# Optimization experiments

Hardware: AMD Instinct MI355X
Metric: run time of the kernel (lower is better)

## Reference

```python
import jax, jax.numpy as jnp
import numpy as np
from jax.scipy.special import logsumexp

UNK_ID = 1
B, T, V = 128, 33, 25000
E, H, D = 256, 256, 512
N, C = 8192, 16384
L = T - 1


def setup_inputs() -> dict:
    key = jax.random.key(0)
    ks = jax.random.split(key, 12)
    input_memories = jax.random.normal(ks[0], (N, D), jnp.float32)
    # each target owns a contiguous block of N//B memories (every segment non-empty)
    origin = jnp.repeat(jnp.arange(B, dtype=jnp.int32), N // B)
    initial_states = jax.random.normal(ks[1], (B, H), jnp.float32)
    target_token_ids = jax.random.randint(ks[2], (B, T), 0, V)
    # copyable elements: pick (memory n, time l); flat idx into [N,L] and [B,L]
    mem_pick = jax.random.randint(ks[3], (C,), 0, N)
    t_pick = jax.random.randint(ks[4], (C,), 0, L)
    copyable_elements_idxs = mem_pick * L + t_pick
    copyable_elements_sample_idxs = origin[mem_pick] * L + t_pick
    target_lengths = jax.random.randint(ks[5], (B,), 1, L + 1)
    emb_weight = 0.02 * jax.random.normal(ks[6], (V, E), jnp.float32)
    gru_w_ih = 0.05 * jax.random.normal(ks[7], (3 * H, E), jnp.float32)
    gru_w_hh = 0.05 * jax.random.normal(ks[8], (3 * H, H), jnp.float32)
    gru_b_ih = jnp.zeros((3 * H,), jnp.float32)
    gru_b_hh = jnp.zeros((3 * H,), jnp.float32)
    w_std_att = 0.05 * jax.random.normal(ks[9], (H, D), jnp.float32)
    w_copy_att = 0.05 * jax.random.normal(ks[10], (H, D), jnp.float32)
    hidden_to_vocab = 0.01 * jax.random.normal(ks[11], (2 * H, E), jnp.float32)
    vocab_bias = jnp.zeros((V,), jnp.float32)
    return dict(input_memories=input_memories, input_memories_origin_idx=origin,
                initial_states=initial_states, target_token_ids=target_token_ids,
                copyable_elements_idxs=copyable_elements_idxs,
                copyable_elements_sample_idxs=copyable_elements_sample_idxs,
                target_lengths=target_lengths, emb_weight=emb_weight,
                gru_w_ih=gru_w_ih, gru_w_hh=gru_w_hh, gru_b_ih=gru_b_ih,
                gru_b_hh=gru_b_hh, w_std_att=w_std_att, w_copy_att=w_copy_att,
                hidden_to_vocab=hidden_to_vocab, vocab_bias=vocab_bias)


def _gru(x, h0, w_ih, w_hh, b_ih, b_hh):
    # x: [B,L,E], h0: [B,H] -> outputs [B,L,H], last state [B,H]
    def step(h, xt):
        gi = xt @ w_ih.T + b_ih
        gh = h @ w_hh.T + b_hh
        ir, iz, inew = jnp.split(gi, 3, axis=-1)
        hr, hz, hnew = jnp.split(gh, 3, axis=-1)
        r = jax.nn.sigmoid(ir + hr)
        z = jax.nn.sigmoid(iz + hz)
        n = jnp.tanh(inew + r * hnew)
        h_next = (1.0 - z) * n + z * h
        return h_next, h_next
    h_last, ys = jax.lax.scan(step, h0, jnp.swapaxes(x, 0, 1))
    return jnp.swapaxes(ys, 0, 1), h_last


def _seg_log_softmax(x, idx, num_seg):
    m = jax.ops.segment_max(x, idx, num_segments=num_seg)
    x_sh = x - m[idx]
    s = jax.ops.segment_sum(jnp.exp(x_sh), idx, num_segments=num_seg)
    return x_sh - jnp.log(s)[idx]


def _seg_logsumexp(x, idx, num_seg):
    m = jax.ops.segment_max(x, idx, num_segments=num_seg)
    m_safe = jnp.where(jnp.isfinite(m), m, 0.0)
    s = jax.ops.segment_sum(jnp.exp(x - m_safe[idx]), idx, num_segments=num_seg)
    return jnp.where(s > 0, jnp.log(jnp.where(s > 0, s, 1.0)) + m_safe, -jnp.inf)


def reference(input_memories, input_memories_origin_idx, initial_states,
              target_token_ids, copyable_elements_idxs,
              copyable_elements_sample_idxs, target_lengths, emb_weight,
              gru_w_ih, gru_w_hh, gru_b_ih, gru_b_hh, w_std_att, w_copy_att,
              hidden_to_vocab, vocab_bias):
    origin = input_memories_origin_idx
    b, t = target_token_ids.shape
    l = t - 1
    tok_in = target_token_ids[:, :-1]
    tok_out = target_token_ids[:, 1:]

    x = emb_weight[tok_in]                                   # [B,L,E]
    out_states, _ = _gru(x, initial_states, gru_w_ih, gru_w_hh, gru_b_ih, gru_b_hh)
    std_reps = input_memories @ w_std_att.T                  # [N,H]
    copy_reps = input_memories @ w_copy_att.T                # [N,H]
    out_per_input = out_states[origin]                       # [N,L,H]
    std_scores = jnp.einsum('nlh,nh->nl', out_per_input, std_reps)
    copy_scores = jnp.einsum('nlh,nh->nl', out_per_input, copy_reps)

    std_logprobs = _seg_log_softmax(std_scores, origin, b)   # [N,L]
    std_mul = jnp.exp(std_logprobs)[:, :, None] * std_reps[:, None, :]
    std_out = jax.ops.segment_sum(std_mul, origin, num_segments=b)  # [B,L,H]

    cat = jnp.concatenate([std_out, out_states], axis=-1)    # [B,L,2H]
    target_scores = (cat @ hidden_to_vocab) @ emb_weight.T + vocab_bias  # [B,L,V]

    total_copy = _seg_logsumexp(copy_scores, origin, b)      # [B,L]
    all_scores = jnp.concatenate([target_scores, total_copy[:, :, None]], axis=-1)
    norm = logsumexp(all_scores, axis=-1)                    # [B,L]
    target_logprobs = target_scores - norm[:, :, None]
    copy_logprobs = copy_scores - norm[origin]               # [N,L]

    num_valid = jax.ops.segment_sum(jnp.ones_like(copyable_elements_sample_idxs),
                                    copyable_elements_sample_idxs,
                                    num_segments=b * l)
    valid_copy = num_valid.reshape(b, l) > 0
    unk_loc = tok_out == UNK_ID
    mask = valid_copy & unk_loc

    gen_lp = jnp.take_along_axis(target_logprobs, tok_out[:, :, None], axis=-1)[..., 0]
    gen_lp = jnp.where(mask, -jnp.inf, gen_lp)

    cc = _seg_logsumexp(copy_logprobs.reshape(-1)[copyable_elements_idxs],
                        copyable_elements_sample_idxs, b * l).reshape(b, l)

    any_lp = logsumexp(jnp.stack([gen_lp, cc]), axis=0)      # [B,L]
    len_mask = (jnp.arange(l)[None, :] < target_lengths[:, None]).astype(jnp.float32)
    per_seq = (any_lp * len_mask).sum(-1) / len_mask.sum(-1)
    return -per_seq.mean()
```

## Files before the change

### kernel.cpp

```cpp
#include <hip/hip_runtime.h>
#include <hip/hip_bf16.h>

#define UNK 1
constexpr int B  = 128, T = 33, V = 25000, E = 256, H = 256, D = 512;
constexpr int N  = 8192, C = 16384, L = 32;
constexpr int BL = B * L;
constexpr int VP = 25088;

typedef __attribute__((ext_vector_type(8))) short bf16x8;
typedef __attribute__((ext_vector_type(4))) float fx4;
typedef unsigned short u16;
typedef unsigned int u32;

__device__ __forceinline__ u16 f2b(float f) {
  u32 u = __float_as_uint(f);
  u += 0x7FFFu + ((u >> 16) & 1u);
  return (u16)(u >> 16);
}
__device__ __forceinline__ float b2f(u16 s) { return __uint_as_float(((u32)s) << 16); }
__device__ __forceinline__ float fsigm(float x) { return 1.f / (1.f + __expf(-x)); }
__device__ __forceinline__ float ftanh(float x) {
  float cx = fminf(fmaxf(x, -15.f), 15.f);
  float e = __expf(2.f * cx);
  return (e - 1.f) / (e + 1.f);
}
__device__ __forceinline__ u32 fkey(float f) {
  u32 b = __float_as_uint(f);
  return (b & 0x80000000u) ? ~b : (b | 0x80000000u);
}
__device__ __forceinline__ float fdec(u32 k) {
  u32 b = (k & 0x80000000u) ? (k & 0x7FFFFFFFu) : ~k;
  return __uint_as_float(b);
}
__device__ __forceinline__ void lcomb(float& M, float& S, float m2, float s2) {
  float Mn = fmaxf(M, m2);
  float a = (S  > 0.f) ? S  * expf(M  - Mn) : 0.f;
  float b = (s2 > 0.f) ? s2 * expf(m2 - Mn) : 0.f;
  M = Mn; S = a + b;
}
__device__ __forceinline__ void gload16(const void* g, void* l) {
  __builtin_amdgcn_global_load_lds(
      (const __attribute__((address_space(1))) void*)g,
      (__attribute__((address_space(3))) void*)l, 16, 0, 0);
}

__device__ __forceinline__ void cvt4_at(const float* in, u16* out, int i) {
  float4 v = *(const float4*)&in[i];
  u16 r[4] = { f2b(v.x), f2b(v.y), f2b(v.z), f2b(v.w) };
  *(ushort4*)&out[i] = *(ushort4*)r;
}

constexpr int PA_EMB = VP * E / 1024;
constexpr int PA_WIH = 768 * 256 / 1024;
constexpr int PA_TOT = PA_EMB + PA_WIH;

__global__ void k_prepA(const float* __restrict__ emb, const float* __restrict__ wih,
                        u16* __restrict__ embb, u16* __restrict__ wihb) {
  int b = blockIdx.x, t = threadIdx.x;
  if (b < PA_EMB) {
    int i = (b * 256 + t) * 4;
    if (i + 3 < V * E) cvt4_at(emb, embb, i);
    else for (int j = 0; j < 4; ++j) embb[i + j] = (i + j < V * E) ? f2b(emb[i + j]) : (u16)0;
    return;
  }
  b -= PA_EMB;
  cvt4_at(wih, wihb, (b * 256 + t) * 4);
}

constexpr int EB_GI  = 192;
constexpr int PBB_MEM = N * D / 1024;
constexpr int PBB_WHH = 192;
constexpr int PBB_WS  = 128;
constexpr int PBB_WC  = 128;
constexpr int PBB_TR  = 512;
constexpr int PBB_INIT= 16;
constexpr int EB_TOT = EB_GI + PBB_MEM + PBB_WHH + PBB_WS + PBB_WC + PBB_TR + PBB_INIT;

__global__ __launch_bounds__(256, 2) void k_embgiB(const int* __restrict__ tok,
    const u16* __restrict__ eb, const u16* __restrict__ wih,
    const float* __restrict__ bih, const float* __restrict__ bhh,
    float* __restrict__ Git,
    const float* __restrict__ mem, const float* __restrict__ whh,
    const float* __restrict__ wstd, const float* __restrict__ wcpy,
    const float* __restrict__ h2v,
    u16* __restrict__ memb, u16* __restrict__ whb,
    u16* __restrict__ wsb, u16* __restrict__ wcb, u16* __restrict__ h2vtb,
    u32* __restrict__ segk, float* __restrict__ segs,
    int* __restrict__ nval, float* __restrict__ lacc) {
  __shared__ __align__(16) u16 As[2][128 * 64];
  __shared__ __align__(16) u16 Bs2[2][128 * 64];
  int e = blockIdx.x, t = threadIdx.x;
  if (e >= EB_GI) {
    int b = e - EB_GI;
    if (b < PBB_MEM) { cvt4_at(mem, memb, (b * 256 + t) * 4); return; }
    b -= PBB_MEM;
    if (b < PBB_WHH) { cvt4_at(whh, whb, (b * 256 + t) * 4); return; }
    b -= PBB_WHH;
    if (b < PBB_WS)  { cvt4_at(wstd, wsb, (b * 256 + t) * 4); return; }
    b -= PBB_WS;
    if (b < PBB_WC)  { cvt4_at(wcpy, wcb, (b * 256 + t) * 4); return; }
    b -= PBB_WC;
    if (b < PBB_TR) {
      int f = b * 256 + t, j = f >> 9, k = f & 511;
      h2vtb[f] = f2b(h2v[k * 256 + j]);
      return;
    }
    b -= PBB_TR;
    int i = b * 256 + t;
    if (i < BL) { segk[i] = 0x007FFFFFu; segs[i] = 0.f; nval[i] = 0; }
    if (i == 0) lacc[0] = 0.f;
    return;
  }
  int m0 = (e & 31) * 128, n0 = (e >> 5) * 128;
  int lane = t & 63, w = t >> 6, wm = w >> 1, wn = w & 1;
  int r16 = lane & 15, hi = lane >> 4;
  char* AsB = (char*)&As[0][0];
  char* BsB = (char*)&Bs2[0][0];
  int tk4[4];
#pragma unroll
  for (int i = 0; i < 4; ++i) {
    int row = (w * 4 + i) * 8 + (lane >> 3);
    int bl = m0 + row;
    tk4[i] = tok[(bl >> 5) * 33 + (bl & 31)];
  }
  fx4 acc[4][4] = {};
  auto stage = [&](int kt, int buf) {
#pragma unroll
    for (int i = 0; i < 4; ++i) {
      int s = (w * 4 + i) * 64 + lane;
      int row = s >> 3, sw = s & 7, c = sw ^ (row & 7);
      gload16(&eb[tk4[i] * 256 + kt * 64 + c * 8], AsB + buf * 16384 + (w * 4 + i) * 1024);
      gload16(&wih[(n0 + row) * 256 + kt * 64 + c * 8], BsB + buf * 16384 + (w * 4 + i) * 1024);
    }
  };
  stage(0, 0);
  for (int kt = 0; kt < 4; ++kt) {
    __syncthreads();
    if (kt < 3) stage(kt + 1, (kt + 1) & 1);
    int buf = kt & 1;
    bf16x8 afr[4][2], bfr[4][2];
#pragma unroll
    for (int mi = 0; mi < 4; ++mi)
#pragma unroll
      for (int kk = 0; kk < 2; ++kk) {
        int row = wm * 64 + mi * 16 + r16, cc = kk * 4 + hi;
        afr[mi][kk] = *(const bf16x8*)(AsB + buf * 16384 + (row * 8 + (cc ^ (row & 7))) * 16);
      }
#pragma unroll
    for (int ni = 0; ni < 4; ++ni)
#pragma unroll
      for (int kk = 0; kk < 2; ++kk) {
        int row = wn * 64 + ni * 16 + r16, cc = kk * 4 + hi;
        bfr[ni][kk] = *(const bf16x8*)(BsB + buf * 16384 + (row * 8 + (cc ^ (row & 7))) * 16);
      }
#pragma unroll
    for (int kk = 0; kk < 2; ++kk)
#pragma unroll
      for (int mi = 0; mi < 4; ++mi)
#pragma unroll
        for (int ni = 0; ni < 4; ++ni)
          acc[mi][ni] = __builtin_amdgcn_mfma_f32_16x16x32_bf16(afr[mi][kk], bfr[ni][kk], acc[mi][ni], 0, 0, 0);
  }
  float bihv[4];
#pragma unroll
  for (int ni = 0; ni < 4; ++ni) {
    int j = n0 + wn * 64 + ni * 16 + r16;
    bihv[ni] = bih[j] + (j < 512 ? bhh[j] : 0.f);
  }
#pragma unroll
  for (int mi = 0; mi < 4; ++mi)
#pragma unroll
    for (int ni = 0; ni < 4; ++ni)
#pragma unroll
      for (int q = 0; q < 4; ++q) {
        int bl = m0 + wm * 64 + mi * 16 + hi * 4 + q;
        int b = bl >> 5, st = bl & 31;
        int j  = n0 + wn * 64 + ni * 16 + r16;
        Git[(((size_t)(b >> 4) * 32 + st) * 768 + j) * 16 + (b & 15)] = acc[mi][ni][q] + bihv[ni];
      }
}

__global__ __launch_bounds__(512, 2) void k_grureps(
    const float* __restrict__ Git, const u16* __restrict__ whb,
    const float* __restrict__ bhh, const float* __restrict__ h0,
    u16* __restrict__ outsb,
    const u16* __restrict__ Am, const u16* __restrict__ wsb,
    const u16* __restrict__ wcb, float* __restrict__ sr, float* __restrict__ cr) {
  __shared__ __align__(16) char smem[147456];
  const int t = threadIdx.x;
  const int w = t >> 6, l = t & 63;

  if (blockIdx.x < 8) {
    u16* nfr = (u16*)smem;
    u16* hbf0 = (u16*)(smem + 131072);
    u16* hbf1 = (u16*)(smem + 131072 + 8192);
    const int lj = l & 15, lk = l >> 4;
    const int b0 = blockIdx.x * 16;

    bf16x8 fr[2][8], fz[2][8];
#pragma unroll
    for (int jh = 0; jh < 2; ++jh)
#pragma unroll
      for (int kc = 0; kc < 8; ++kc) {
        int jr = w * 32 + jh * 16 + lj;
        int k0 = kc * 32 + lk * 8;
        fr[jh][kc] = *(const bf16x8*)&whb[(0 * 256 + jr) * 256 + k0];
        fz[jh][kc] = *(const bf16x8*)&whb[(1 * 256 + jr) * 256 + k0];
        int4 nv = *(const int4*)&whb[(2 * 256 + jr) * 256 + k0];
        *(int4*)&nfr[((w * 16 + jh * 8 + kc) * 64 + l) * 8] = nv;
      }
    float bN[2];
#pragma unroll
    for (int jh = 0; jh < 2; ++jh) bN[jh] = bhh[512 + w * 32 + jh * 16 + lj];
    float hst[2][4];
#pragma unroll
    for (int jh = 0; jh < 2; ++jh)
#pragma unroll
      for (int q = 0; q < 4; ++q) {
        int m = lk * 4 + q, j = w * 32 + jh * 16 + lj;
        hst[jh][q] = h0[(b0 + m) * 256 + j];
        hbf0[m * 256 + (((j >> 3) ^ (m & 7)) * 8) + (j & 7)] = f2b(hst[jh][q]);
      }
    __syncthreads();

    for (int st = 0; st < 32; ++st) {
      const float* gb = Git + (size_t)(blockIdx.x * 32 + st) * 768 * 16;
      fx4 grz[4];
#pragma unroll
      for (int g = 0; g < 2; ++g)
#pragma unroll
        for (int jh = 0; jh < 2; ++jh)
          grz[g * 2 + jh] = *(const fx4*)&gb[(g * 256 + w * 32 + jh * 16 + lj) * 16 + lk * 4];
      fx4 gn[2];
      fx4 accR[2] = {}, accZ[2] = {}, accN[2] = {};
      const u16* hb = (st & 1) ? hbf1 : hbf0;
#pragma unroll
      for (int kc = 0; kc < 8; ++kc) {
        int k8 = kc * 4 + lk;
        bf16x8 a = *(const bf16x8*)&hb[lj * 256 + ((k8 ^ (lj & 7)) * 8)];
        bf16x8 nf0 = *(const bf16x8*)&nfr[((w * 16 + 0 + kc) * 64 + l) * 8];
        bf16x8 nf1 = *(const bf16x8*)&nfr[((w * 16 + 8 + kc) * 64 + l) * 8];
        accR[0] = __builtin_amdgcn_mfma_f32_16x16x32_bf16(a, fr[0][kc], accR[0], 0, 0, 0);
        accR[1] = __builtin_amdgcn_mfma_f32_16x16x32_bf16(a, fr[1][kc], accR[1], 0, 0, 0);
        accZ[0] = __builtin_amdgcn_mfma_f32_16x16x32_bf16(a, fz[0][kc], accZ[0], 0, 0, 0);
        accZ[1] = __builtin_amdgcn_mfma_f32_16x16x32_bf16(a, fz[1][kc], accZ[1], 0, 0, 0);
        accN[0] = __builtin_amdgcn_mfma_f32_16x16x32_bf16(a, nf0, accN[0], 0, 0, 0);
        accN[1] = __builtin_amdgcn_mfma_f32_16x16x32_bf16(a, nf1, accN[1], 0, 0, 0);
        if (kc == 5) {
#pragma unroll
          for (int jh = 0; jh < 2; ++jh)
            gn[jh] = *(const fx4*)&gb[(2 * 256 + w * 32 + jh * 16 + lj) * 16 + lk * 4];
        }
      }
      u16* hw = (st & 1) ? hbf0 : hbf1;
#pragma unroll
      for (int jh = 0; jh < 2; ++jh)
#pragma unroll
        for (int q = 0; q < 4; ++q) {
          float r = fsigm(grz[jh][q] + accR[jh][q]);
          float z = fsigm(grz[2 + jh][q] + accZ[jh][q]);
          float n = ftanh(gn[jh][q] + r * (accN[jh][q] + bN[jh]));
          float hn = (1.f - z) * n + z * hst[jh][q];
          hst[jh][q] = hn;
          int m = lk * 4 + q, j = w * 32 + jh * 16 + lj;
          u16 hbv = f2b(hn);
          hw[m * 256 + (((j >> 3) ^ (m & 7)) * 8) + (j & 7)] = hbv;
          outsb[((size_t)(b0 + m) * 32 + st) * 256 + j] = hbv;
        }
      __syncthreads();
    }
    return;
  }

  int rb = blockIdx.x - 8;
  int m0 = (rb >> 1) * 128, sn = rb & 1;
  const u16* Bsrc = sn ? wcb : wsb;
  int grp = w >> 2, wg = w & 3, wm = wg >> 1, wn = wg & 1;
  int jb = grp * 128;
  int lane = l, r16 = lane & 15, hi = lane >> 4;
  char* AsB = smem;
  char* BsB = smem + 32768 + grp * 32768;
  fx4 acc[4][4] = {};
  auto stage = [&](int kt, int buf) {
    if (grp == 0) {
#pragma unroll
      for (int i = 0; i < 4; ++i) {
        int s = (wg * 4 + i) * 64 + lane;
        int row = s >> 3, sw = s & 7, c = sw ^ (row & 7);
        gload16(&Am[(m0 + row) * 512 + kt * 64 + c * 8], AsB + buf * 16384 + (wg * 4 + i) * 1024);
        gload16(&Bsrc[(0 + row) * 512 + kt * 64 + c * 8], (smem + 32768) + buf * 16384 + (wg * 4 + i) * 1024);
      }
    } else {
#pragma unroll
      for (int i = 0; i < 4; ++i) {
        int s = (wg * 4 + i) * 64 + lane;
        int row = s >> 3, sw = s & 7, c = sw ^ (row & 7);
        gload16(&Bsrc[(128 + row) * 512 + kt * 64 + c * 8], (smem + 65536) + buf * 16384 + (wg * 4 + i) * 1024);
      }
    }
  };
  stage(0, 0);
  for (int kt = 0; kt < 8; ++kt) {
    __syncthreads();
    if (kt < 7) stage(kt + 1, (kt + 1) & 1);
    int buf = kt & 1;
    bf16x8 afr[4][2], bfr[4][2];
#pragma unroll
    for (int mi = 0; mi < 4; ++mi)
#pragma unroll
      for (int kk = 0; kk < 2; ++kk) {
        int row = wm * 64 + mi * 16 + r16, cc = kk * 4 + hi;
        afr[mi][kk] = *(const bf16x8*)(AsB + buf * 16384 + (row * 8 + (cc ^ (row & 7))) * 16);
      }
#pragma unroll
    for (int ni = 0; ni < 4; ++ni)
#pragma unroll
      for (int kk = 0; kk < 2; ++kk) {
        int row = wn * 64 + ni * 16 + r16, cc = kk * 4 + hi;
        bfr[ni][kk] = *(const bf16x8*)(BsB + buf * 16384 + (row * 8 + (cc ^ (row & 7))) * 16);
      }
#pragma unroll
    for (int kk = 0; kk < 2; ++kk)
#pragma unroll
      for (int mi = 0; mi < 4; ++mi)
#pragma unroll
        for (int ni = 0; ni < 4; ++ni)
          acc[mi][ni] = __builtin_amdgcn_mfma_f32_16x16x32_bf16(afr[mi][kk], bfr[ni][kk], acc[mi][ni], 0, 0, 0);
  }
#pragma unroll
  for (int mi = 0; mi < 4; ++mi)
#pragma unroll
    for (int ni = 0; ni < 4; ++ni)
#pragma unroll
      for (int q = 0; q < 4; ++q) {
        int mr = m0 + wm * 64 + mi * 16 + hi * 4 + q;
        int j  = sn * 256 + jb + wn * 64 + ni * 16 + r16;
        float vv = acc[mi][ni][q];
        if (j < 256) sr[mr * 256 + j] = vv; else cr[mr * 256 + (j - 256)] = vv;
      }
}

__global__ void k_scores(const u16* __restrict__ outsb, const float* __restrict__ sr,
                         const float* __restrict__ cr, float* __restrict__ ss,
                         float* __restrict__ cs) {
  __shared__ float os[32][257];
  int b = blockIdx.x >> 2, nc = blockIdx.x & 3, t = threadIdx.x;
  for (int i = 0; i < 8; ++i) {
    int q = t + 256 * i, row = q >> 6, c4 = q & 63;
    ushort4 v = *(const ushort4*)&outsb[(b * 32 + row) * 256 + c4 * 4];
    os[row][c4 * 4] = b2f(v.x); os[row][c4 * 4 + 1] = b2f(v.y);
    os[row][c4 * 4 + 2] = b2f(v.z); os[row][c4 * 4 + 3] = b2f(v.w);
  }
  __syncthreads();
  int l = t & 31, g = t >> 5;
  for (int rep = 0; rep < 2; ++rep) {
    int n = b * 64 + nc * 16 + g + rep * 8;
    float a = 0.f, c = 0.f;
    for (int k4 = 0; k4 < 64; ++k4) {
      float4 s4 = *(const float4*)&sr[n * 256 + k4 * 4];
      float4 c4v = *(const float4*)&cr[n * 256 + k4 * 4];
      float o0 = os[l][k4 * 4], o1 = os[l][k4 * 4 + 1];
      float o2 = os[l][k4 * 4 + 2], o3 = os[l][k4 * 4 + 3];
      a = fmaf(o0, s4.x, a); a = fmaf(o1, s4.y, a);
      a = fmaf(o2, s4.z, a); a = fmaf(o3, s4.w, a);
      c = fmaf(o0, c4v.x, c); c = fmaf(o1, c4v.y, c);
      c = fmaf(o2, c4v.z, c); c = fmaf(o3, c4v.w, c);
    }
    ss[n * 32 + l] = a; cs[n * 32 + l] = c;
  }
}

__global__ void k_smx(const float* __restrict__ ss, const float* __restrict__ cs,
                      const float* __restrict__ sr, u16* __restrict__ sob,
                      float* __restrict__ tc) {
  __shared__ float wst[64][33];
  __shared__ float wcp[64][33];
  int b = blockIdx.x, t = threadIdx.x;
  for (int i = 0; i < 8; ++i) {
    int q = t + 256 * i;
    wst[q >> 5][q & 31] = ss[b * 2048 + q];
    wcp[q >> 5][q & 31] = cs[b * 2048 + q];
  }
  __syncthreads();
  if (t < 32) {
    int l = t; float m = -1e30f;
    for (int n = 0; n < 64; ++n) m = fmaxf(m, wst[n][l]);
    float s = 0.f;
    for (int n = 0; n < 64; ++n) s += expf(wst[n][l] - m);
    float inv = 1.f / s;
    for (int n = 0; n < 64; ++n) wst[n][l] = expf(wst[n][l] - m) * inv;
  } else if (t < 64) {
    int l = t - 32; float m = -1e30f;
    for (int n = 0; n < 64; ++n) m = fmaxf(m, wcp[n][l]);
    float s = 0.f;
    for (int n = 0; n < 64; ++n) s += expf(wcp[n][l] - m);
    tc[b * 32 + l] = m + logf(s);
  }
  __syncthreads();
  float acc[32] = {};
  for (int n = 0; n < 64; ++n) {
    float v = sr[(b * 64 + n) * 256 + t];
#pragma unroll
    for (int l = 0; l < 32; ++l) acc[l] = fmaf(wst[n][l], v, acc[l]);
  }
  for (int l = 0; l < 32; ++l) sob[(b * 32 + l) * 256 + t] = f2b(acc[l]);
}

__global__ __launch_bounds__(256, 2) void k_projM(const u16* __restrict__ sob,
    const u16* __restrict__ outsb, const u16* __restrict__ h2vtb,
    u16* __restrict__ pb) {
  __shared__ __align__(16) u16 As[2][128 * 64];
  __shared__ __align__(16) u16 Bs2[2][128 * 64];
  int t = threadIdx.x;
  int m0 = blockIdx.x * 128, n0 = blockIdx.y * 128;
  int lane = t & 63, w = t >> 6, wm = w >> 1, wn = w & 1;
  int r16 = lane & 15, hi = lane >> 4;
  char* AsB = (char*)&As[0][0];
  char* BsB = (char*)&Bs2[0][0];
  fx4 acc[4][4] = {};
  auto stage = [&](int kt, int buf) {
    const u16* Asrc = (kt < 4) ? sob : outsb;
    int ko = (kt & 3) * 64;
#pragma unroll
    for (int i = 0; i < 4; ++i) {
      int s = (w * 4 + i) * 64 + lane;
      int row = s >> 3, sw = s & 7, c = sw ^ (row & 7);
      gload16(&Asrc[(m0 + row) * 256 + ko + c * 8], AsB + buf * 16384 + (w * 4 + i) * 1024);
      gload16(&h2vtb[(n0 + row) * 512 + kt * 64 + c * 8], BsB + buf * 16384 + (w * 4 + i) * 1024);
    }
  };
  stage(0, 0);
  for (int kt = 0; kt < 8; ++kt) {
    __syncthreads();
    if (kt < 7) stage(kt + 1, (kt + 1) & 1);
    int buf = kt & 1;
    bf16x8 afr[4][2], bfr[4][2];
#pragma unroll
    for (int mi = 0; mi < 4; ++mi)
#pragma unroll
      for (int kk = 0; kk < 2; ++kk) {
        int row = wm * 64 + mi * 16 + r16, cc = kk * 4 + hi;
        afr[mi][kk] = *(const bf16x8*)(AsB + buf * 16384 + (row * 8 + (cc ^ (row & 7))) * 16);
      }
#pragma unroll
    for (int ni = 0; ni < 4; ++ni)
#pragma unroll
      for (int kk = 0; kk < 2; ++kk) {
        int row = wn * 64 + ni * 16 + r16, cc = kk * 4 + hi;
        bfr[ni][kk] = *(const bf16x8*)(BsB + buf * 16384 + (row * 8 + (cc ^ (row & 7))) * 16);
      }
#pragma unroll
    for (int kk = 0; kk < 2; ++kk)
#pragma unroll
      for (int mi = 0; mi < 4; ++mi)
#pragma unroll
        for (int ni = 0; ni < 4; ++ni)
          acc[mi][ni] = __builtin_amdgcn_mfma_f32_16x16x32_bf16(afr[mi][kk], bfr[ni][kk], acc[mi][ni], 0, 0, 0);
  }
#pragma unroll
  for (int mi = 0; mi < 4; ++mi)
#pragma unroll
    for (int ni = 0; ni < 4; ++ni)
#pragma unroll
      for (int q = 0; q < 4; ++q) {
        int mr = m0 + wm * 64 + mi * 16 + hi * 4 + q;
        int j  = n0 + wn * 64 + ni * 16 + r16;
        pb[mr * 256 + j] = f2b(acc[mi][ni][q]);
      }
}

__global__ void k_gen(const u16* __restrict__ pb, const u16* __restrict__ eb,
                      const int* __restrict__ tok, const float* __restrict__ vb,
                      float* __restrict__ gs) {
  int w = threadIdx.x >> 6, lane = threadIdx.x & 63;
  int row = blockIdx.x * 4 + w;
  int b = row >> 5, l = row & 31;
  int tk = tok[b * 33 + l + 1];
  float s = 0.f;
#pragma unroll
  for (int i = 0; i < 4; ++i) {
    int k = lane * 4 + i;
    s += b2f(pb[row * 256 + k]) * b2f(eb[tk * 256 + k]);
  }
#pragma unroll
  for (int d = 1; d < 64; d <<= 1) s += __shfl_xor(s, d);
  if (lane == 0) gs[row] = s + vb[tk];
}

__global__ __launch_bounds__(256, 1) void k_gemm(const u16* __restrict__ A,
    const u16* __restrict__ Bm, const float* __restrict__ vb,
    float* __restrict__ parts) {
  __shared__ __align__(16) u16 Bs[2][128 * 256];
  __shared__ float red[2][128];
  int t = threadIdx.x;
  int vr = blockIdx.x & 7, mch = blockIdx.x >> 3;
  int m0 = mch * 128;
  int c0 = vr * 24 + min(vr, 4);
  int cn = 24 + (vr < 4 ? 1 : 0);
  int lane = t & 63, w = t >> 6, wm = w >> 1, wn = w & 1;
  int r16 = lane & 15, hi = lane >> 4;
  char* BsB = (char*)&Bs[0][0];
  const char* Bb = (const char*)Bm;

  bf16x8 af[4][8];
#pragma unroll
  for (int mi = 0; mi < 4; ++mi)
#pragma unroll
    for (int ks = 0; ks < 8; ++ks)
      af[mi][ks] = *(const bf16x8*)&A[(m0 + wm * 64 + mi * 16 + r16) * 256 + ks * 32 + hi * 8];

  int soff[16];
#pragma unroll
  for (int i = 0; i < 16; ++i) {
    int row = (w * 16 + i) * 2 + (lane >> 5);
    int gs = lane & 31;
    int gsrc = (gs & ~7) | ((gs & 7) ^ (row & 7));
    soff[i] = row * 512 + gsrc * 16;
  }

  float Sa[4][4] = {};

#define STAGE(CG, BUF)                                                        \
  {                                                                           \
    _Pragma("unroll")                                                         \
    for (int i = 0; i < 16; ++i)                                              \
      gload16(Bb + (CG) * 65536 + soff[i],                                    \
              BsB + (BUF) * 65536 + w * 16384 + i * 1024);                    \
  }

  STAGE(c0, 0);
  for (int c = 0; c < cn; ++c) {
    int cg = c0 + c;
    __syncthreads();
    if (c + 1 < cn) STAGE(cg + 1, (c + 1) & 1);
    int buf = c & 1;
    fx4 acc[4][4] = {};
#pragma unroll
    for (int ks = 0; ks < 8; ++ks)
#pragma unroll
      for (int ni = 0; ni < 4; ++ni) {
        int row = wn * 64 + ni * 16 + r16;
        int g = ks * 4 + hi;
        int gp = (g & ~7) | ((g & 7) ^ (row & 7));
        bf16x8 bfv = *(const bf16x8*)(BsB + buf * 65536 + row * 512 + gp * 16);
#pragma unroll
        for (int mi = 0; mi < 4; ++mi)
          acc[mi][ni] = __builtin_amdgcn_mfma_f32_16x16x32_bf16(af[mi][ks], bfv, acc[mi][ni], 0, 0, 0);
      }
    float bias[4];
#pragma unroll
    for (int ni = 0; ni < 4; ++ni) {
      int v = cg * 128 + wn * 64 + ni * 16 + r16;
      bias[ni] = (v < V) ? vb[v] : -1e30f;
    }
#pragma unroll
    for (int mi = 0; mi < 4; ++mi)
#pragma unroll
      for (int q = 0; q < 4; ++q) {
        float e = 0.f;
#pragma unroll
        for (int ni = 0; ni < 4; ++ni)
          e += __expf(acc[mi][ni][q] + bias[ni]);
        Sa[mi][q] += e;
      }
  }
#undef STAGE

#pragma unroll
  for (int mi = 0; mi < 4; ++mi)
#pragma unroll
    for (int q = 0; q < 4; ++q) {
      float s = Sa[mi][q];
#pragma unroll
      for (int d = 1; d < 16; d <<= 1) s += __shfl_xor(s, d);
      Sa[mi][q] = s;
    }
  if (r16 == 0) {
#pragma unroll
    for (int mi = 0; mi < 4; ++mi)
#pragma unroll
      for (int q = 0; q < 4; ++q)
        red[wn][wm * 64 + mi * 16 + hi * 4 + q] = Sa[mi][q];
  }
  __syncthreads();
  if (t < 128)
    parts[(m0 + t) * 8 + vr] = red[0][t] + red[1][t];
}

__global__ void k_seg(const int* __restrict__ idx, const int* __restrict__ sid,
                      const float* __restrict__ cs, u32* __restrict__ sk,
                      int* __restrict__ nv) {
  int c = blockIdx.x * 256 + threadIdx.x;
  if (c < C) {
    int s = sid[c];
    atomicMax(&sk[s], fkey(cs[idx[c]]));
    atomicAdd(&nv[s], 1);
  }
}
__global__ void k_segsum(const int* __restrict__ idx, const int* __restrict__ sid,
                         const float* __restrict__ cs, const u32* __restrict__ sk,
                         float* __restrict__ ssum) {
  int c = blockIdx.x * 256 + threadIdx.x;
  if (c < C) {
    int s = sid[c];
    atomicAdd(&ssum[s], __expf(cs[idx[c]] - fdec(sk[s])));
  }
}

__global__ void k_final(const float* __restrict__ parts, const float* __restrict__ tc,
                        const float* __restrict__ gs, const u32* __restrict__ sk,
                        const float* __restrict__ ssum, const int* __restrict__ nv,
                        const int* __restrict__ tok, const int* __restrict__ tlen,
                        float* __restrict__ lacc) {
  int i = blockIdx.x * 256 + threadIdx.x;
  int b = i >> 5, l = i & 31;
  float S = 0.f;
#pragma unroll
  for (int r = 0; r < 8; ++r) S += parts[i * 8 + r];
  float M = 0.f, Ss = S;
  lcomb(M, Ss, tc[i], 1.f);
  float nrm = M + logf(Ss);
  int tk = tok[b * 33 + l + 1];
  float glp = gs[i] - nrm;
  int cnt = nv[i];
  if (cnt > 0 && tk == UNK) glp = -INFINITY;
  float cc = (cnt > 0) ? (logf(ssum[i]) + fdec(sk[i]) - nrm) : -INFINITY;
  float m = fmaxf(glp, cc);
  float any = (m == -INFINITY) ? -INFINITY : m + logf(expf(glp - m) + expf(cc - m));
  float oa = (l < tlen[b]) ? any : 0.f;
#pragma unroll
  for (int d = 1; d < 32; d <<= 1) oa += __shfl_xor(oa, d);
  if (l == 0) atomicAdd(lacc, oa / (float)tlen[b]);
}

__global__ void k_loss(const float* __restrict__ lacc, float* __restrict__ out) {
  out[0] = -lacc[0] / 128.f;
}

extern "C" void kernel_launch(void* const* d_in, const int* in_sizes, int n_in,
                              void* d_out, int out_size, void* d_ws, size_t ws_size,
                              hipStream_t stream) {
  const float* mem  = (const float*)d_in[0];
  const float* h0   = (const float*)d_in[2];
  const int*   tok  = (const int*)d_in[3];
  const int*   cidx = (const int*)d_in[4];
  const int*   csid = (const int*)d_in[5];
  const int*   tlen = (const int*)d_in[6];
  const float* emb  = (const float*)d_in[7];
  const float* wih  = (const float*)d_in[8];
  const float* whh  = (const float*)d_in[9];
  const float* bih  = (const float*)d_in[10];
  const float* bhh  = (const float*)d_in[11];
  const float* wstd = (const float*)d_in[12];
  const float* wcpy = (const float*)d_in[13];
  const float* h2v  = (const float*)d_in[14];
  const float* vb   = (const float*)d_in[15];

  char* ws = (char*)d_ws;
  size_t off = 0;
  auto alloc = [&](size_t bytes) -> char* {
    char* p = ws + off;
    off = (off + bytes + 255) & ~(size_t)255;
    return p;
  };
  u16*    embb  = (u16*)   alloc((size_t)VP * E * 2);
  u16*    memb  = (u16*)   alloc((size_t)N * D * 2);
  u16*    wihb  = (u16*)   alloc(768 * 256 * 2);
  u16*    whb   = (u16*)   alloc(768 * 256 * 2);
  u16*    wsb   = (u16*)   alloc(256 * 512 * 2);
  u16*    wcb   = (u16*)   alloc(256 * 512 * 2);
  u16*    h2vtb = (u16*)   alloc(256 * 512 * 2);
  float*  Git   = (float*) alloc((size_t)BL * 768 * 4);
  u16*    outsb = (u16*)   alloc((size_t)BL * 256 * 2);
  u16*    stdob = (u16*)   alloc((size_t)BL * 256 * 2);
  float*  sreps = (float*) alloc((size_t)N * 256 * 4);
  float*  creps = (float*) alloc((size_t)N * 256 * 4);
  float*  sscr  = (float*) alloc((size_t)N * 32 * 4);
  float*  cscr  = (float*) alloc((size_t)N * 32 * 4);
  float*  tcopy = (float*) alloc(BL * 4);
  u16*    projb = (u16*)   alloc((size_t)BL * 256 * 2);
  float*  parts = (float*) alloc((size_t)BL * 8 * 4);
  float*  gens  = (float*) alloc(BL * 4);
  u32*    segk  = (u32*)   alloc(BL * 4);
  float*  segs  = (float*) alloc(BL * 4);
  int*    nval  = (int*)   alloc(BL * 4);
  float*  lacc  = (float*) alloc(256);
  (void)ws_size; (void)in_sizes; (void)n_in; (void)out_size;

  k_prepA<<<PA_TOT, 256, 0, stream>>>(emb, wih, embb, wihb);
  k_embgiB<<<EB_TOT, 256, 0, stream>>>(tok, embb, wihb, bih, bhh, Git,
                                       mem, whh, wstd, wcpy, h2v,
                                       memb, whb, wsb, wcb, h2vtb,
                                       segk, segs, nval, lacc);
  k_grureps<<<136, 512, 0, stream>>>(Git, whb, bhh, h0, outsb,
                                     memb, wsb, wcb, sreps, creps);
  k_scores<<<512, 256, 0, stream>>>(outsb, sreps, creps, sscr, cscr);
  k_seg<<<64, 256, 0, stream>>>(cidx, csid, cscr, segk, nval);
  k_segsum<<<64, 256, 0, stream>>>(cidx, csid, cscr, segk, segs);
  k_smx<<<128, 256, 0, stream>>>(sscr, cscr, sreps, stdob, tcopy);
  k_projM<<<dim3(32, 2), 256, 0, stream>>>(stdob, outsb, h2vtb, projb);
  k_gen<<<1024, 256, 0, stream>>>(projb, embb, tok, vb, gens);
  k_gemm<<<256, 256, 0, stream>>>(projb, embb, vb, parts);
  k_final<<<16, 256, 0, stream>>>(parts, tcopy, gens, segk, segs, nval, tok, tlen, lacc);
  k_loss<<<1, 1, 0, stream>>>(lacc, (float*)d_out);
}
```

Before: 284.8 us.

## Fuse embedding/W_ih bf16 conversion into input-gate GEMM kernel, drop prep launch

Removes the separate k_prepA launch by folding the embedding-table bf16 conversion into the combined prep/GEMM kernel's extra blocks. The input-gate GEMM now reads fp32 embeddings and W_ih directly, converts them to bf16 in registers, and stores them to LDS, replacing the async global-to-LDS loads of pre-converted bf16 data. This saves one kernel launch and the dependency between the two kernels. The cost is twice the global bytes per GEMM tile, plus synchronous loads, conversion ALU work and reordered barriers.

Result: no change. 284.6 us (-0.1%).

```diff
diff --git a/kernel.cpp b/kernel.cpp
--- a/kernel.cpp
+++ b/kernel.cpp
@@ -50,40 +50,24 @@
   *(ushort4*)&out[i] = *(ushort4*)r;
 }
 
-constexpr int PA_EMB = VP * E / 1024;
-constexpr int PA_WIH = 768 * 256 / 1024;
-constexpr int PA_TOT = PA_EMB + PA_WIH;
-
-__global__ void k_prepA(const float* __restrict__ emb, const float* __restrict__ wih,
-                        u16* __restrict__ embb, u16* __restrict__ wihb) {
-  int b = blockIdx.x, t = threadIdx.x;
-  if (b < PA_EMB) {
-    int i = (b * 256 + t) * 4;
-    if (i + 3 < V * E) cvt4_at(emb, embb, i);
-    else for (int j = 0; j < 4; ++j) embb[i + j] = (i + j < V * E) ? f2b(emb[i + j]) : (u16)0;
-    return;
-  }
-  b -= PA_EMB;
-  cvt4_at(wih, wihb, (b * 256 + t) * 4);
-}
-
-constexpr int EB_GI  = 192;
-constexpr int PBB_MEM = N * D / 1024;
-constexpr int PBB_WHH = 192;
-constexpr int PBB_WS  = 128;
-constexpr int PBB_WC  = 128;
-constexpr int PBB_TR  = 512;
-constexpr int PBB_INIT= 16;
-constexpr int EB_TOT = EB_GI + PBB_MEM + PBB_WHH + PBB_WS + PBB_WC + PBB_TR + PBB_INIT;
-
-__global__ __launch_bounds__(256, 2) void k_embgiB(const int* __restrict__ tok,
-    const u16* __restrict__ eb, const u16* __restrict__ wih,
+constexpr int EB_GI   = 192;
+constexpr int P2_EMB  = VP * E / 1024;
+constexpr int P2_MEM  = N * D / 1024;
+constexpr int P2_WHH  = 192;
+constexpr int P2_WS   = 128;
+constexpr int P2_WC   = 128;
+constexpr int P2_TR   = 512;
+constexpr int P2_INIT = 16;
+constexpr int EB2_TOT = EB_GI + P2_EMB + P2_MEM + P2_WHH + P2_WS + P2_WC + P2_TR + P2_INIT;
+
+__global__ __launch_bounds__(256, 2) void k_embgiB2(const int* __restrict__ tok,
+    const float* __restrict__ emb, const float* __restrict__ wih,
     const float* __restrict__ bih, const float* __restrict__ bhh,
     float* __restrict__ Git,
     const float* __restrict__ mem, const float* __restrict__ whh,
     const float* __restrict__ wstd, const float* __restrict__ wcpy,
     const float* __restrict__ h2v,
-    u16* __restrict__ memb, u16* __restrict__ whb,
+    u16* __restrict__ embb, u16* __restrict__ memb, u16* __restrict__ whb,
     u16* __restrict__ wsb, u16* __restrict__ wcb, u16* __restrict__ h2vtb,
     u32* __restrict__ segk, float* __restrict__ segs,
     int* __restrict__ nval, float* __restrict__ lacc) {
@@ -92,20 +76,27 @@
   int e = blockIdx.x, t = threadIdx.x;
   if (e >= EB_GI) {
     int b = e - EB_GI;
-    if (b < PBB_MEM) { cvt4_at(mem, memb, (b * 256 + t) * 4); return; }
-    b -= PBB_MEM;
-    if (b < PBB_WHH) { cvt4_at(whh, whb, (b * 256 + t) * 4); return; }
-    b -= PBB_WHH;
-    if (b < PBB_WS)  { cvt4_at(wstd, wsb, (b * 256 + t) * 4); return; }
-    b -= PBB_WS;
-    if (b < PBB_WC)  { cvt4_at(wcpy, wcb, (b * 256 + t) * 4); return; }
-    b -= PBB_WC;
-    if (b < PBB_TR) {
+    if (b < P2_EMB) {
+      int i = (b * 256 + t) * 4;
+      if (i + 3 < V * E) cvt4_at(emb, embb, i);
+      else for (int j = 0; j < 4; ++j) embb[i + j] = (i + j < V * E) ? f2b(emb[i + j]) : (u16)0;
+      return;
+    }
+    b -= P2_EMB;
+    if (b < P2_MEM) { cvt4_at(mem, memb, (b * 256 + t) * 4); return; }
+    b -= P2_MEM;
+    if (b < P2_WHH) { cvt4_at(whh, whb, (b * 256 + t) * 4); return; }
+    b -= P2_WHH;
+    if (b < P2_WS)  { cvt4_at(wstd, wsb, (b * 256 + t) * 4); return; }
+    b -= P2_WS;
+    if (b < P2_WC)  { cvt4_at(wcpy, wcb, (b * 256 + t) * 4); return; }
+    b -= P2_WC;
+    if (b < P2_TR) {
       int f = b * 256 + t, j = f >> 9, k = f & 511;
       h2vtb[f] = f2b(h2v[k * 256 + j]);
       return;
     }
-    b -= PBB_TR;
+    b -= P2_TR;
     int i = b * 256 + t;
     if (i < BL) { segk[i] = 0x007FFFFFu; segs[i] = 0.f; nval[i] = 0; }
     if (i == 0) lacc[0] = 0.f;
@@ -127,16 +118,23 @@
   auto stage = [&](int kt, int buf) {
 #pragma unroll
     for (int i = 0; i < 4; ++i) {
-      int s = (w * 4 + i) * 64 + lane;
-      int row = s >> 3, sw = s & 7, c = sw ^ (row & 7);
-      gload16(&eb[tk4[i] * 256 + kt * 64 + c * 8], AsB + buf * 16384 + (w * 4 + i) * 1024);
-      gload16(&wih[(n0 + row) * 256 + kt * 64 + c * 8], BsB + buf * 16384 + (w * 4 + i) * 1024);
+      int row = (w * 4 + i) * 8 + (lane >> 3);
+      int c = (lane & 7) ^ (row & 7);
+      float4 a0 = *(const float4*)&emb[tk4[i] * 256 + kt * 64 + c * 8];
+      float4 a1 = *(const float4*)&emb[tk4[i] * 256 + kt * 64 + c * 8 + 4];
+      __align__(16) u16 ra[8] = { f2b(a0.x), f2b(a0.y), f2b(a0.z), f2b(a0.w),
+                                  f2b(a1.x), f2b(a1.y), f2b(a1.z), f2b(a1.w) };
+      *(int4*)(AsB + buf * 16384 + (w * 4 + i) * 1024 + lane * 16) = *(const int4*)ra;
+      float4 b0 = *(const float4*)&wih[(n0 + row) * 256 + kt * 64 + c * 8];
+      float4 b1 = *(const float4*)&wih[(n0 + row) * 256 + kt * 64 + c * 8 + 4];
+      __align__(16) u16 rb[8] = { f2b(b0.x), f2b(b0.y), f2b(b0.z), f2b(b0.w),
+                                  f2b(b1.x), f2b(b1.y), f2b(b1.z), f2b(b1.w) };
+      *(int4*)(BsB + buf * 16384 + (w * 4 + i) * 1024 + lane * 16) = *(const int4*)rb;
     }
   };
   stage(0, 0);
+  __syncthreads();
   for (int kt = 0; kt < 4; ++kt) {
-    __syncthreads();
-    if (kt < 3) stage(kt + 1, (kt + 1) & 1);
     int buf = kt & 1;
     bf16x8 afr[4][2], bfr[4][2];
 #pragma unroll
@@ -153,6 +151,9 @@
         int row = wn * 64 + ni * 16 + r16, cc = kk * 4 + hi;
         bfr[ni][kk] = *(const bf16x8*)(BsB + buf * 16384 + (row * 8 + (cc ^ (row & 7))) * 16);
       }
+    if (kt < 3) {
+      stage(kt + 1, (kt + 1) & 1);
+    }
 #pragma unroll
     for (int kk = 0; kk < 2; ++kk)
 #pragma unroll
@@ -160,6 +161,7 @@
 #pragma unroll
         for (int ni = 0; ni < 4; ++ni)
           acc[mi][ni] = __builtin_amdgcn_mfma_f32_16x16x32_bf16(afr[mi][kk], bfr[ni][kk], acc[mi][ni], 0, 0, 0);
+    __syncthreads();
   }
   float bihv[4];
 #pragma unroll
@@ -665,7 +667,6 @@
   };
   u16*    embb  = (u16*)   alloc((size_t)VP * E * 2);
   u16*    memb  = (u16*)   alloc((size_t)N * D * 2);
-  u16*    wihb  = (u16*)   alloc(768 * 256 * 2);
   u16*    whb   = (u16*)   alloc(768 * 256 * 2);
   u16*    wsb   = (u16*)   alloc(256 * 512 * 2);
   u16*    wcb   = (u16*)   alloc(256 * 512 * 2);
@@ -687,11 +688,10 @@
   float*  lacc  = (float*) alloc(256);
   (void)ws_size; (void)in_sizes; (void)n_in; (void)out_size;
 
-  k_prepA<<<PA_TOT, 256, 0, stream>>>(emb, wih, embb, wihb);
-  k_embgiB<<<EB_TOT, 256, 0, stream>>>(tok, embb, wihb, bih, bhh, Git,
-                                       mem, whh, wstd, wcpy, h2v,
-                                       memb, whb, wsb, wcb, h2vtb,
-                                       segk, segs, nval, lacc);
+  k_embgiB2<<<EB2_TOT, 256, 0, stream>>>(tok, emb, wih, bih, bhh, Git,
+                                         mem, whh, wstd, wcpy, h2v,
+                                         embb, memb, whb, wsb, wcb, h2vtb,
+                                         segk, segs, nval, lacc);
   k_grureps<<<136, 512, 0, stream>>>(Git, whb, bhh, h0, outsb,
                                      memb, wsb, wcb, sreps, creps);
   k_scores<<<512, 256, 0, stream>>>(outsb, sreps, creps, sscr, cscr);
```
